# Optimization experiments

Measured on AMD Instinct MI355X. Metric: run time of the kernel, lower is better.

## Reference

```python
import jax, jax.numpy as jnp
import numpy as np

B, F, T, C, H, HH = 16384, 2048, 64, 32, 24, 48  # batch, features, n_tails, cluster_size, tail_hidden, head_hidden


def setup_inputs() -> dict:
    key = jax.random.key(0)
    ks = jax.random.split(key, 8)
    x = jax.random.normal(ks[0], (B, F), dtype=jnp.float32)
    clusters = jnp.arange(T * C, dtype=jnp.int32).reshape(T, C)  # equal-size partition of features
    # tied autoencoder weights: encoder = x @ W + hb, decoder = h @ W.T + vb
    Wt = jax.random.normal(ks[1], (T, C, H), dtype=jnp.float32) * 0.1
    hb = jax.random.normal(ks[2], (T, H), dtype=jnp.float32) * 0.1
    vb = jax.random.normal(ks[3], (T, C), dtype=jnp.float32) * 0.1
    Wh = jax.random.normal(ks[4], (T, HH), dtype=jnp.float32) * 0.1
    hbh = jax.random.normal(ks[5], (HH,), dtype=jnp.float32) * 0.1
    vbh = jax.random.normal(ks[6], (T,), dtype=jnp.float32) * 0.1
    return {"x": x, "clusters": clusters, "Wt": Wt, "hb": hb, "vb": vb,
            "Wh": Wh, "hbh": hbh, "vbh": vbh}


def reference(x, clusters, Wt, hb, vb, Wh, hbh, vbh):
    # gather all clusters in one shot: [B, T, C]
    xg = x[:, clusters]
    # batched tiny autoencoders (encode then decode with tied weight W)
    h = jnp.einsum('btc,tch->bth', xg, Wt) + hb[None, :, :]
    out = jnp.einsum('bth,tch->btc', h, Wt) + vb[None, :, :]
    # per-tail log-RMSE over (batch, cluster) elements -> [T]
    rmse = jnp.sqrt(jnp.mean(jnp.square(out - xg), axis=(0, 2)))
    tails = jnp.log(rmse)
    # head autoencoder on the tail-loss vector
    hh = tails @ Wh + hbh          # [HH]
    head_out = hh @ Wh.T + vbh     # [T]
    return head_out, tails
```

## Files before the change

kernel.cpp:

```cpp
#include <hip/hip_runtime.h>
#include <cstddef>

#define B_  16384
#define F_  2048
#define T_  64
#define C_  32
#define H_  24
#define HH_ 48
#define THR 256
#define ROWS_BLK 1024
#define NCHUNK (B_ / ROWS_BLK)
#define GRID_  (T_ * NCHUNK)
#define SL_STRIDE 72

typedef __attribute__((ext_vector_type(8))) short  short8;
typedef __attribute__((ext_vector_type(4))) float  floatx4;

__device__ __forceinline__ short f2bf(float f) {
    union { float f; unsigned u; } v; v.f = f;
    unsigned r = v.u + 0x7FFFu + ((v.u >> 16) & 1u);
    return (short)(r >> 16);
}

__global__ __launch_bounds__(THR) void kitnet_main(
    const float* __restrict__ x, const int* __restrict__ clusters,
    const float* __restrict__ Wt, const float* __restrict__ hb,
    const float* __restrict__ vb, float* __restrict__ partial)
{
    __shared__ __align__(16) float WL[C_ * H_];
    __shared__ __align__(16) float GL[H_ * H_];
    __shared__ __align__(16) float w2L[C_];
    __shared__ __align__(16) float dL[H_];
    __shared__ __align__(16) float hbL[H_];
    __shared__ float k0L;
    __shared__ int   colsL[C_];
    __shared__ int   contigS;
    __shared__ float wsum[4];
    __shared__ __align__(16) short Sl[8 * 16 * SL_STRIDE];

    const int tid   = threadIdx.x;
    const int t     = blockIdx.x >> 4;
    const int chunk = blockIdx.x & (NCHUNK - 1);
    const int b0    = chunk * ROWS_BLK;

    for (int i = tid; i < C_ * H_; i += THR) WL[i] = Wt[t * C_ * H_ + i];
    if (tid < H_) hbL[tid] = hb[t * H_ + tid];
    if (tid < C_) colsL[tid] = clusters[t * C_ + tid];
    __syncthreads();

    if (tid < C_) {
        float a = vb[t * C_ + tid];
        #pragma unroll
        for (int j = 0; j < H_; ++j) a += WL[tid * H_ + j] * hbL[j];
        w2L[tid] = a;
    }
    if (tid == 0) {
        int ok = (colsL[0] & 3) == 0;
        for (int c = 1; c < C_; ++c) ok &= (colsL[c] == colsL[0] + c);
        contigS = ok;
    }
    __syncthreads();

    for (int idx = tid; idx < H_ * H_; idx += THR) {
        const int i = idx / H_, j = idx - i * H_;
        float a = 0.f;
        #pragma unroll
        for (int c = 0; c < C_; ++c) a += WL[c * H_ + i] * WL[c * H_ + j];
        GL[idx] = (i == j) ? a - 2.f : a;
    }
    if (tid < H_) {
        float a = 0.f;
        #pragma unroll
        for (int c = 0; c < C_; ++c) a += w2L[c] * WL[c * H_ + tid];
        dL[tid] = 2.f * a;
    }
    if (tid == THR - 1) {
        float a = 0.f;
        for (int c = 0; c < C_; ++c) a += w2L[c] * w2L[c];
        k0L = a;
    }
    __syncthreads();

    const int lane = tid & 63;
    const int wid  = tid >> 6;
    const int m    = lane & 15;
    const int quad = lane >> 4;

    short8 bw0, bw1, gg0, gg1;
    float  m2w[8];
    #pragma unroll
    for (int j = 0; j < 8; ++j) {
        const int k = quad * 8 + j;
        bw0[j] = f2bf(WL[k * H_ + m]);
        bw1[j] = (m < 8) ? f2bf(WL[k * H_ + 16 + m]) : (short)0;
        gg0[j] = (k < H_) ? f2bf(GL[k * H_ + m]) : (short)0;
        gg1[j] = (k < H_ && m < 8) ? f2bf(GL[k * H_ + 16 + m]) : (short)0;
        m2w[j] = -2.f * w2L[k];
    }
    const float d0 = dL[m];
    const float d1 = (m < 8) ? dL[16 + m] : 0.f;

    short* sl0 = &Sl[(wid * 2 + 0) * 16 * SL_STRIDE];
    short* sl1 = &Sl[(wid * 2 + 1) * 16 * SL_STRIDE];
    const int contig = contigS;
    const int col0   = colsL[0];
    float err = 0.f, errB = 0.f;

#define PROCESS16(XA, XB, SLP, ERR)                                           \
    {                                                                         \
        const float xv_[8] = {XA.x, XA.y, XA.z, XA.w, XB.x, XB.y, XB.z, XB.w};\
        short8 af;                                                            \
        _Pragma("unroll")                                                     \
        for (int j = 0; j < 8; ++j) {                                         \
            ERR += xv_[j] * xv_[j] + xv_[j] * m2w[j];                         \
            af[j] = f2bf(xv_[j]);                                             \
        }                                                                     \
        const floatx4 z_ = {0.f, 0.f, 0.f, 0.f};                              \
        floatx4 S0 = __builtin_amdgcn_mfma_f32_16x16x32_bf16(af, bw0, z_, 0, 0, 0); \
        floatx4 S1 = __builtin_amdgcn_mfma_f32_16x16x32_bf16(af, bw1, z_, 0, 0, 0); \
        _Pragma("unroll")                                                     \
        for (int r = 0; r < 4; ++r) {                                         \
            (SLP)[(quad * 4 + r) * SL_STRIDE + m]      = f2bf(S0[r]);         \
            (SLP)[(quad * 4 + r) * SL_STRIDE + 16 + m] = f2bf(S1[r]);         \
        }                                                                     \
        short8 sf = *(const short8*)&(SLP)[m * SL_STRIDE + quad * 8];         \
        floatx4 Q0 = __builtin_amdgcn_mfma_f32_16x16x32_bf16(sf, gg0, z_, 0, 0, 0); \
        floatx4 Q1 = __builtin_amdgcn_mfma_f32_16x16x32_bf16(sf, gg1, z_, 0, 0, 0); \
        _Pragma("unroll")                                                     \
        for (int r = 0; r < 4; ++r)                                           \
            ERR += (Q0[r] + d0) * S0[r] + (Q1[r] + d1) * S1[r];               \
    }

    if (contig) {
        const float* xbase = x + (size_t)(b0 + wid * 256 + m) * F_ + col0 + quad * 8;
        float4 a0 = *(const float4*)xbase;
        float4 c0 = *(const float4*)(xbase + 4);
        float4 a1 = *(const float4*)(xbase + (size_t)16 * F_);
        float4 c1 = *(const float4*)(xbase + (size_t)16 * F_ + 4);
        for (int gp = 0; gp < 8; ++gp) {
            const float4 xa0 = a0, xc0 = c0, xa1 = a1, xc1 = c1;
            if (gp < 7) {
                const float* nx = xbase + (size_t)(2 * gp + 2) * 16 * F_;
                a0 = *(const float4*)nx;
                c0 = *(const float4*)(nx + 4);
                a1 = *(const float4*)(nx + (size_t)16 * F_);
                c1 = *(const float4*)(nx + (size_t)16 * F_ + 4);
            }
            PROCESS16(xa0, xc0, sl0, err)
            PROCESS16(xa1, xc1, sl1, errB)
        }
    } else {
        for (int g = 0; g < 16; ++g) {
            const size_t rb = (size_t)(b0 + wid * 256 + g * 16 + m) * F_;
            float xf[8];
            #pragma unroll
            for (int j = 0; j < 8; ++j) xf[j] = x[rb + colsL[quad * 8 + j]];
            float4 xa = {xf[0], xf[1], xf[2], xf[3]};
            float4 xc = {xf[4], xf[5], xf[6], xf[7]};
            PROCESS16(xa, xc, sl0, err)
        }
    }
#undef PROCESS16
    err += errB;

    #pragma unroll
    for (int off = 32; off > 0; off >>= 1) err += __shfl_down(err, off, 64);
    if (lane == 0) wsum[wid] = err;
    __syncthreads();
    if (tid == 0)
        partial[blockIdx.x] = wsum[0] + wsum[1] + wsum[2] + wsum[3]
                            + (float)ROWS_BLK * k0L;
}

__global__ __launch_bounds__(64) void kitnet_head(
    const float* __restrict__ partial, const float* __restrict__ Wh,
    const float* __restrict__ hbh, const float* __restrict__ vbh,
    float* __restrict__ out)
{
    __shared__ float tl[T_];
    __shared__ float hhL[HH_];
    const int tid = threadIdx.x;

    float sse = 0.f;
    #pragma unroll
    for (int c = 0; c < NCHUNK; ++c) sse += partial[tid * NCHUNK + c];

    const float tail = 0.5f * logf(sse * (1.0f / ((float)B_ * (float)C_)));
    tl[tid] = tail;
    out[T_ + tid] = tail;
    __syncthreads();

    if (tid < HH_) {
        float acc = hbh[tid];
        #pragma unroll 8
        for (int t = 0; t < T_; ++t) acc += tl[t] * Wh[t * HH_ + tid];
        hhL[tid] = acc;
    }
    __syncthreads();

    float ho = vbh[tid];
    #pragma unroll 8
    for (int j = 0; j < HH_; ++j) ho += hhL[j] * Wh[tid * HH_ + j];
    out[tid] = ho;
}

extern "C" void kernel_launch(void* const* d_in, const int* in_sizes, int n_in,
                              void* d_out, int out_size, void* d_ws, size_t ws_size,
                              hipStream_t stream)
{
    const float* x        = (const float*)d_in[0];
    const int*   clusters = (const int*)  d_in[1];
    const float* Wt       = (const float*)d_in[2];
    const float* hb       = (const float*)d_in[3];
    const float* vb       = (const float*)d_in[4];
    const float* Wh       = (const float*)d_in[5];
    const float* hbh      = (const float*)d_in[6];
    const float* vbh      = (const float*)d_in[7];
    float* out     = (float*)d_out;
    float* partial = (float*)d_ws;

    kitnet_main<<<dim3(GRID_), dim3(THR), 0, stream>>>(x, clusters, Wt, hb, vb, partial);
    kitnet_head<<<dim3(1), dim3(64), 0, stream>>>(partial, Wh, hbh, vbh, out);
}
```

Baseline: 237.9 us.

## Accumulate hidden Gram matrix via MFMA instead of per-row quadratic form through LDS

The per-row quadratic term S·G·S is replaced by accumulating the batch Gram matrix S^T S across row groups with MFMAs, then contracting it with G once per wave at the end. This removes the LDS round-trip used to transpose S and the two G-MFMAs per group. The linear term is folded into column sums of S. Rows per block are halved to double the grid, and launch bounds request higher occupancy. This relies on the bf16 rounding of S in the Gram accumulation being accurate enough.

```diff
diff --git a/kernel.cpp b/kernel.cpp
--- a/kernel.cpp
+++ b/kernel.cpp
@@ -8,13 +8,13 @@
 #define H_  24
 #define HH_ 48
 #define THR 256
-#define ROWS_BLK 1024
+#define ROWS_BLK 512
 #define NCHUNK (B_ / ROWS_BLK)
 #define GRID_  (T_ * NCHUNK)
-#define SL_STRIDE 72
 
 typedef __attribute__((ext_vector_type(8))) short  short8;
 typedef __attribute__((ext_vector_type(4))) float  floatx4;
+typedef __attribute__((ext_vector_type(4))) int    intx4;
 
 __device__ __forceinline__ short f2bf(float f) {
     union { float f; unsigned u; } v; v.f = f;
@@ -22,7 +22,15 @@
     return (short)(r >> 16);
 }
 
-__global__ __launch_bounds__(THR) void kitnet_main(
+__device__ __forceinline__ int pk2bf(float lo, float hi) {
+    union { float f; unsigned u; } a, b;
+    a.f = lo; b.f = hi;
+    unsigned ra = (a.u + 0x7FFFu + ((a.u >> 16) & 1u)) >> 16;
+    unsigned rb = (b.u + 0x7FFFu + ((b.u >> 16) & 1u)) & 0xFFFF0000u;
+    return (int)(ra | rb);
+}
+
+__global__ __launch_bounds__(THR, 6) void kitnet_main(
     const float* __restrict__ x, const int* __restrict__ clusters,
     const float* __restrict__ Wt, const float* __restrict__ hb,
     const float* __restrict__ vb, float* __restrict__ partial)
@@ -36,10 +44,9 @@
     __shared__ int   colsL[C_];
     __shared__ int   contigS;
     __shared__ float wsum[4];
-    __shared__ __align__(16) short Sl[8 * 16 * SL_STRIDE];
 
     const int tid   = threadIdx.x;
-    const int t     = blockIdx.x >> 4;
+    const int t     = blockIdx.x >> 5;
     const int chunk = blockIdx.x & (NCHUNK - 1);
     const int b0    = chunk * ROWS_BLK;
 
@@ -86,82 +93,115 @@
     const int m    = lane & 15;
     const int quad = lane >> 4;
 
-    short8 bw0, bw1, gg0, gg1;
+    short8 bw0, bw1;
     float  m2w[8];
     #pragma unroll
     for (int j = 0; j < 8; ++j) {
         const int k = quad * 8 + j;
         bw0[j] = f2bf(WL[k * H_ + m]);
         bw1[j] = (m < 8) ? f2bf(WL[k * H_ + 16 + m]) : (short)0;
-        gg0[j] = (k < H_) ? f2bf(GL[k * H_ + m]) : (short)0;
-        gg1[j] = (k < H_ && m < 8) ? f2bf(GL[k * H_ + 16 + m]) : (short)0;
         m2w[j] = -2.f * w2L[k];
     }
     const float d0 = dL[m];
     const float d1 = (m < 8) ? dL[16 + m] : 0.f;
 
-    short* sl0 = &Sl[(wid * 2 + 0) * 16 * SL_STRIDE];
-    short* sl1 = &Sl[(wid * 2 + 1) * 16 * SL_STRIDE];
     const int contig = contigS;
     const int col0   = colsL[0];
-    float err = 0.f, errB = 0.f;
-
-#define PROCESS16(XA, XB, SLP, ERR)                                           \
+
+    const floatx4 z4 = {0.f, 0.f, 0.f, 0.f};
+    floatx4 Mll = z4, Mlh = z4, Mhh = z4;
+    floatx4 cs0 = z4, cs1 = z4;
+    float err = 0.f;
+    int pA0, pA1, qA0, qA1, pB0, pB1, qB0, qB1;
+
+#define GROUPG(XA, XB, P0, P1, Q0, Q1)                                        \
     {                                                                         \
         const float xv_[8] = {XA.x, XA.y, XA.z, XA.w, XB.x, XB.y, XB.z, XB.w};\
         short8 af;                                                            \
         _Pragma("unroll")                                                     \
         for (int j = 0; j < 8; ++j) {                                         \
-            ERR += xv_[j] * xv_[j] + xv_[j] * m2w[j];                         \
+            err += xv_[j] * xv_[j] + xv_[j] * m2w[j];                         \
             af[j] = f2bf(xv_[j]);                                             \
         }                                                                     \
-        const floatx4 z_ = {0.f, 0.f, 0.f, 0.f};                              \
-        floatx4 S0 = __builtin_amdgcn_mfma_f32_16x16x32_bf16(af, bw0, z_, 0, 0, 0); \
-        floatx4 S1 = __builtin_amdgcn_mfma_f32_16x16x32_bf16(af, bw1, z_, 0, 0, 0); \
-        _Pragma("unroll")                                                     \
-        for (int r = 0; r < 4; ++r) {                                         \
-            (SLP)[(quad * 4 + r) * SL_STRIDE + m]      = f2bf(S0[r]);         \
-            (SLP)[(quad * 4 + r) * SL_STRIDE + 16 + m] = f2bf(S1[r]);         \
-        }                                                                     \
-        short8 sf = *(const short8*)&(SLP)[m * SL_STRIDE + quad * 8];         \
-        floatx4 Q0 = __builtin_amdgcn_mfma_f32_16x16x32_bf16(sf, gg0, z_, 0, 0, 0); \
-        floatx4 Q1 = __builtin_amdgcn_mfma_f32_16x16x32_bf16(sf, gg1, z_, 0, 0, 0); \
-        _Pragma("unroll")                                                     \
-        for (int r = 0; r < 4; ++r)                                           \
-            ERR += (Q0[r] + d0) * S0[r] + (Q1[r] + d1) * S1[r];               \
+        floatx4 S0 = __builtin_amdgcn_mfma_f32_16x16x32_bf16(af, bw0, z4, 0, 0, 0); \
+        floatx4 S1 = __builtin_amdgcn_mfma_f32_16x16x32_bf16(af, bw1, z4, 0, 0, 0); \
+        cs0 += S0; cs1 += S1;                                                 \
+        P0 = pk2bf(S0[0], S0[1]); P1 = pk2bf(S0[2], S0[3]);                   \
+        Q0 = pk2bf(S1[0], S1[1]); Q1 = pk2bf(S1[2], S1[3]);                   \
+    }
+
+#define PAIRC                                                                 \
+    {                                                                         \
+        intx4 ia, ib;                                                         \
+        ia[0] = pA0; ia[1] = pA1; ia[2] = pB0; ia[3] = pB1;                   \
+        ib[0] = qA0; ib[1] = qA1; ib[2] = qB0; ib[3] = qB1;                   \
+        const short8 SA = __builtin_bit_cast(short8, ia);                     \
+        const short8 SB = __builtin_bit_cast(short8, ib);                     \
+        Mll = __builtin_amdgcn_mfma_f32_16x16x32_bf16(SA, SA, Mll, 0, 0, 0);  \
+        Mlh = __builtin_amdgcn_mfma_f32_16x16x32_bf16(SA, SB, Mlh, 0, 0, 0);  \
+        Mhh = __builtin_amdgcn_mfma_f32_16x16x32_bf16(SB, SB, Mhh, 0, 0, 0);  \
     }
 
     if (contig) {
-        const float* xbase = x + (size_t)(b0 + wid * 256 + m) * F_ + col0 + quad * 8;
-        float4 a0 = *(const float4*)xbase;
-        float4 c0 = *(const float4*)(xbase + 4);
-        float4 a1 = *(const float4*)(xbase + (size_t)16 * F_);
-        float4 c1 = *(const float4*)(xbase + (size_t)16 * F_ + 4);
-        for (int gp = 0; gp < 8; ++gp) {
-            const float4 xa0 = a0, xc0 = c0, xa1 = a1, xc1 = c1;
-            if (gp < 7) {
-                const float* nx = xbase + (size_t)(2 * gp + 2) * 16 * F_;
-                a0 = *(const float4*)nx;
-                c0 = *(const float4*)(nx + 4);
-                a1 = *(const float4*)(nx + (size_t)16 * F_);
-                c1 = *(const float4*)(nx + (size_t)16 * F_ + 4);
-            }
-            PROCESS16(xa0, xc0, sl0, err)
-            PROCESS16(xa1, xc1, sl1, errB)
+        const float* xbase = x + (size_t)(b0 + wid * 128 + m) * F_ + col0 + quad * 8;
+        float4 na = *(const float4*)xbase;
+        float4 nc = *(const float4*)(xbase + 4);
+        #pragma unroll
+        for (int g = 0; g < 8; g += 2) {
+            const float4 xa0 = na, xc0 = nc;
+            {
+                const float* s1 = xbase + (size_t)(g + 1) * 16 * F_;
+                na = *(const float4*)s1;
+                nc = *(const float4*)(s1 + 4);
+            }
+            GROUPG(xa0, xc0, pA0, pA1, qA0, qA1)
+            const float4 xa1 = na, xc1 = nc;
+            if (g < 6) {
+                const float* s2 = xbase + (size_t)(g + 2) * 16 * F_;
+                na = *(const float4*)s2;
+                nc = *(const float4*)(s2 + 4);
+            }
+            GROUPG(xa1, xc1, pB0, pB1, qB0, qB1)
+            PAIRC
         }
     } else {
-        for (int g = 0; g < 16; ++g) {
-            const size_t rb = (size_t)(b0 + wid * 256 + g * 16 + m) * F_;
-            float xf[8];
+        for (int g = 0; g < 8; g += 2) {
+            const size_t rb0 = (size_t)(b0 + wid * 128 + g * 16 + m) * F_;
+            const size_t rb1 = rb0 + (size_t)16 * F_;
+            float xf[8], yf[8];
             #pragma unroll
-            for (int j = 0; j < 8; ++j) xf[j] = x[rb + colsL[quad * 8 + j]];
-            float4 xa = {xf[0], xf[1], xf[2], xf[3]};
-            float4 xc = {xf[4], xf[5], xf[6], xf[7]};
-            PROCESS16(xa, xc, sl0, err)
+            for (int j = 0; j < 8; ++j) {
+                xf[j] = x[rb0 + colsL[quad * 8 + j]];
+                yf[j] = x[rb1 + colsL[quad * 8 + j]];
+            }
+            const float4 xa0 = {xf[0], xf[1], xf[2], xf[3]};
+            const float4 xc0 = {xf[4], xf[5], xf[6], xf[7]};
+            const float4 xa1 = {yf[0], yf[1], yf[2], yf[3]};
+            const float4 xc1 = {yf[4], yf[5], yf[6], yf[7]};
+            GROUPG(xa0, xc0, pA0, pA1, qA0, qA1)
+            GROUPG(xa1, xc1, pB0, pB1, qB0, qB1)
+            PAIRC
         }
     }
-#undef PROCESS16
-    err += errB;
+#undef GROUPG
+#undef PAIRC
+
+    {
+        const int i0 = quad * 4;
+        float eg = 0.f;
+        #pragma unroll
+        for (int r = 0; r < 4; ++r) {
+            eg += GL[(i0 + r) * H_ + m] * Mll[r];
+            if (m < 8) {
+                eg += 2.f * GL[(i0 + r) * H_ + 16 + m] * Mlh[r];
+                if (i0 + r < 8)
+                    eg += GL[(16 + i0 + r) * H_ + 16 + m] * Mhh[r];
+            }
+        }
+        err += eg;
+        err += (cs0[0] + cs0[1] + cs0[2] + cs0[3]) * d0;
+        if (m < 8) err += (cs1[0] + cs1[1] + cs1[2] + cs1[3]) * d1;
+    }
 
     #pragma unroll
     for (int off = 32; off > 0; off >>= 1) err += __shfl_down(err, off, 64);
@@ -182,7 +222,7 @@
     const int tid = threadIdx.x;
 
     float sse = 0.f;
-    #pragma unroll
+    #pragma unroll 8
     for (int c = 0; c < NCHUNK; ++c) sse += partial[tid * NCHUNK + c];
 
     const float tail = 0.5f * logf(sse * (1.0f / ((float)B_ * (float)C_)));
```

Measured after the change: 215.0 us. -9.6%, faster.
